# Optimization experiments

Measured on AMD Instinct MI355X. Metric: run time of the kernel, lower is better.

The kernel has to match this reference:

```python
import jax, jax.numpy as jnp
import numpy as np

NUM_NODES_G1 = 60000
NUM_NODES_G2 = 50000
NUM_REL = 16
NUM_BASES = 4
DIM = 128  # node_dim == hidden_dim == final_dim
L_COMMON = 100


def _concept_layer(x, edge_index):
    # Gather-based concept propagation: x_i <- x_i + mean_{j in N(i)} x_j
    src, dst = edge_index[0], edge_index[1]
    n = x.shape[0]
    agg = jax.ops.segment_sum(x[src], dst, num_segments=n)
    deg = jax.ops.segment_sum(jnp.ones((src.shape[0],), x.dtype), dst, num_segments=n)
    return x + agg / jnp.clip(deg, 1.0)[:, None]


def _rgcn_layer(x, edge_index, edge_type, basis, comp, root, bias):
    # Basis-decomposed RGCN: out_i = x_i @ root + bias + sum_r (1/|N_i^r|) sum_{j in N_i^r} x_j @ W_r,
    # W_r = sum_b comp[r,b] * basis[b]. Reorder: scatter comp-weighted x[src] per basis, then one GEMM per basis.
    src, dst = edge_index[0], edge_index[1]
    n = x.shape[0]
    e = src.shape[0]
    seg = dst * NUM_REL + edge_type  # per-(node, relation) bucket
    cnt = jax.ops.segment_sum(jnp.ones((e,), x.dtype), seg, num_segments=n * NUM_REL)
    norm = 1.0 / jnp.clip(cnt, 1.0)
    coef = comp[edge_type] * norm[seg][:, None]  # [E, B]
    xsrc = x[src]  # [E, D] -- dominant gather traffic
    out = x @ root + bias
    for b in range(NUM_BASES):  # small fixed loop over bases
        agg_b = jax.ops.segment_sum(xsrc * coef[:, b:b + 1], dst, num_segments=n)
        out = out + agg_b @ basis[b]
    return out


def setup_inputs() -> dict:
    key = jax.random.key(0)
    ks = jax.random.split(key, 16)
    e2, e1 = 800000, 800000
    return {
        "edge_index_g2": jax.random.randint(ks[0], (2, e2), 0, NUM_NODES_G2),
        "edge_type_g2": jax.random.randint(ks[1], (e2,), 0, NUM_REL),
        "edge_index_g1": jax.random.randint(ks[2], (2, e1), 0, NUM_NODES_G1),
        "left_common": jax.random.randint(ks[3], (L_COMMON,), 0, NUM_NODES_G1),
        "all_node_embedding": jax.random.normal(ks[4], (NUM_NODES_G1, DIM), jnp.float32),
        "basis1": jax.random.normal(ks[5], (NUM_BASES, DIM, DIM), jnp.float32) * 0.05,
        "comp1": jax.random.normal(ks[6], (NUM_REL, NUM_BASES), jnp.float32),
        "root1": jax.random.normal(ks[7], (DIM, DIM), jnp.float32) * 0.05,
        "bias1": jnp.zeros((DIM,), jnp.float32),
        "basis2": jax.random.normal(ks[8], (NUM_BASES, DIM, DIM), jnp.float32) * 0.05,
        "comp2": jax.random.normal(ks[9], (NUM_REL, NUM_BASES), jnp.float32),
        "root2": jax.random.normal(ks[10], (DIM, DIM), jnp.float32) * 0.05,
        "bias2": jnp.zeros((DIM,), jnp.float32),
        "weights": jax.random.uniform(ks[11], (DIM, 1), jnp.float32),
    }


def reference(edge_index_g2, edge_type_g2, edge_index_g1, left_common,
              all_node_embedding, basis1, comp1, root1, bias1,
              basis2, comp2, root2, bias2, weights):
    x_g1 = jax.nn.relu(_concept_layer(all_node_embedding, edge_index_g1))
    x = x_g1[:NUM_NODES_G2]
    x = _rgcn_layer(x, edge_index_g2, edge_type_g2, basis1, comp1, root1, bias1)
    x = jax.nn.relu(x)  # relu_use == 1
    x_g2 = _rgcn_layer(x, edge_index_g2, edge_type_g2, basis2, comp2, root2, bias2)
    ty = x_g1[left_common]  # [L, D]
    # mul_def outer elementwise product followed by matmul with weights collapses to one contraction:
    # logits[n,l] = sum_d x_g2[n,d] * ty[l,d] * w[d]
    logits = jnp.einsum('nd,ld,d->nl', x_g2, ty, weights[:, 0])
    return jax.nn.softmax(logits, axis=1)
```

## Files before the change

### kernel.cpp

```cpp
#include <hip/hip_runtime.h>
#include <hip/hip_bf16.h>
#include <math.h>

#define N1 60000
#define N2 50000
#define DIM 128
#define NREL 16
#define NB 4
#define LCOM 100
#define LPAD 112

typedef __attribute__((ext_vector_type(8))) short short8;
typedef __attribute__((ext_vector_type(4))) float f32x4;
typedef __attribute__((ext_vector_type(4))) _Float16 half4;

__device__ __forceinline__ float bf2f(unsigned short u) {
    union { unsigned int i; float f; } c; c.i = ((unsigned int)u) << 16; return c.f;
}
__device__ __forceinline__ unsigned short f2bf(float f) {
    union { float f; unsigned int i; } c; c.f = f;
    unsigned int r = c.i + 0x7FFF + ((c.i >> 16) & 1);
    return (unsigned short)(r >> 16);
}
__device__ __forceinline__ void split8(float4 a, float4 b, short8& h, short8& l) {
    float f[8] = {a.x, a.y, a.z, a.w, b.x, b.y, b.z, b.w};
#pragma unroll
    for (int j = 0; j < 8; j++) {
        unsigned short hh = f2bf(f[j]);
        h[j] = (short)hh;
        l[j] = (short)f2bf(f[j] - bf2f(hh));
    }
}

__global__ __launch_bounds__(256) void k_prelude(
        const int* __restrict__ ei1, int E1, int* __restrict__ deg1, int HB1,
        const int* __restrict__ ei2, int E2, int* __restrict__ deg2, int HB2,
        const float* __restrict__ root1, const float* __restrict__ basis1,
        unsigned short* __restrict__ Wh1, unsigned short* __restrict__ Wl1,
        const float* __restrict__ root2, const float* __restrict__ basis2,
        unsigned short* __restrict__ Wh2, unsigned short* __restrict__ Wl2, int PB,
        const float* __restrict__ emb, _Float16* __restrict__ embh, int n4) {
    int b = blockIdx.x;
    if (b < HB1) {
        int e0 = b * 1024 + threadIdx.x;
#pragma unroll
        for (int j = 0; j < 4; j++) {
            int e = e0 + j * 256;
            if (e < E1) atomicAdd(deg1 + ei1[E1 + e], 1);
        }
    } else if (b < HB1 + HB2) {
        int e0 = (b - HB1) * 1024 + threadIdx.x;
#pragma unroll
        for (int j = 0; j < 4; j++) {
            int e = e0 + j * 256;
            if (e < E2) atomicAdd(deg2 + ei2[E2 + e], 1);
        }
    } else if (b < HB1 + HB2 + PB) {
        int t = (b - HB1 - HB2) * 256 + threadIdx.x;
        if (t < 2 * 640 * 128) {
            int which = t >= 640 * 128;
            int tt = which ? t - 640 * 128 : t;
            const float* root = which ? root2 : root1;
            const float* basis = which ? basis2 : basis1;
            unsigned short* Wh = which ? Wh2 : Wh1;
            unsigned short* Wl = which ? Wl2 : Wl1;
            int k = tt >> 7, n = tt & 127;
            float v = (k < 128) ? root[k * 128 + n] : basis[(k - 128) * 128 + n];
            unsigned short h = f2bf(v);
            Wh[n * 640 + k] = h;
            Wl[n * 640 + k] = f2bf(v - bf2f(h));
        }
    } else {
        int i = (b - HB1 - HB2 - PB) * 256 + threadIdx.x;
        if (i < n4) {
            float4 v = ((const float4*)emb)[i];
            half4 o = {(_Float16)v.x, (_Float16)v.y, (_Float16)v.z, (_Float16)v.w};
            ((half4*)embh)[i] = o;
        }
    }
}

__global__ __launch_bounds__(256) void k_scan_p1m(const int* __restrict__ inA, int nA, int nbA,
                                                  int* __restrict__ bsumA,
                                                  const int* __restrict__ inB, int nB,
                                                  int* __restrict__ bsumB) {
    __shared__ int red[256];
    const int* in; int n; int* bsum; int b;
    if ((int)blockIdx.x < nbA) { in = inA; n = nA; bsum = bsumA; b = blockIdx.x; }
    else { in = inB; n = nB; bsum = bsumB; b = blockIdx.x - nbA; }
    int base = b * 1024;
    int tid = threadIdx.x;
    int s = 0;
#pragma unroll
    for (int j = 0; j < 4; j++) {
        int i = base + tid * 4 + j;
        if (i < n) s += in[i];
    }
    red[tid] = s;
    __syncthreads();
    for (int d = 128; d; d >>= 1) {
        if (tid < d) red[tid] += red[tid + d];
        __syncthreads();
    }
    if (tid == 0) bsum[b] = red[0];
}

__global__ __launch_bounds__(64) void k_scan_p2m(const int* __restrict__ bsumA, int* __restrict__ boffA,
                                                 int* __restrict__ offA, int nbA, int nA,
                                                 const int* __restrict__ bsumB, int* __restrict__ boffB,
                                                 int* __restrict__ offB, int nbB, int nB) {
    __shared__ int s[64];
    const int* bsum; int* boff; int* off; int nb; int n;
    if (blockIdx.x == 0) { bsum = bsumA; boff = boffA; off = offA; nb = nbA; n = nA; }
    else { bsum = bsumB; boff = boffB; off = offB; nb = nbB; n = nB; }
    int tid = threadIdx.x;
    int v = (tid < nb) ? bsum[tid] : 0;
    s[tid] = v;
    __syncthreads();
    for (int d = 1; d < 64; d <<= 1) {
        int t = (tid >= d) ? s[tid - d] : 0;
        __syncthreads();
        s[tid] += t;
        __syncthreads();
    }
    if (tid < nb) boff[tid] = s[tid] - v;
    if (tid == 63) off[n] = s[63];
}

__global__ __launch_bounds__(256) void k_scan_p3m(const int* __restrict__ inA, const int* __restrict__ boffA,
                                                  int* __restrict__ offA, int* __restrict__ curA,
                                                  int nA, int nbA,
                                                  const int* __restrict__ inB, const int* __restrict__ boffB,
                                                  int* __restrict__ offB, int* __restrict__ curB, int nB) {
    __shared__ int red[256];
    const int* in; const int* boff; int* off; int* cur; int n; int b;
    if ((int)blockIdx.x < nbA) { in = inA; boff = boffA; off = offA; cur = curA; n = nA; b = blockIdx.x; }
    else { in = inB; boff = boffB; off = offB; cur = curB; n = nB; b = blockIdx.x - nbA; }
    int base = b * 1024;
    int tid = threadIdx.x;
    int v[4];
    int s = 0;
#pragma unroll
    for (int j = 0; j < 4; j++) {
        int i = base + tid * 4 + j;
        v[j] = (i < n) ? in[i] : 0;
        s += v[j];
    }
    red[tid] = s;
    __syncthreads();
    for (int d = 1; d < 256; d <<= 1) {
        int t = (tid >= d) ? red[tid - d] : 0;
        __syncthreads();
        red[tid] += t;
        __syncthreads();
    }
    int run = boff[b] + red[tid] - s;
#pragma unroll
    for (int j = 0; j < 4; j++) {
        int i = base + tid * 4 + j;
        if (i < n) {
            off[i] = run; cur[i] = run;
            run += v[j];
        }
    }
}

__global__ void k_scat1(const int* __restrict__ ei, int E, int* __restrict__ cur,
                        int* __restrict__ elist) {
    int e0 = blockIdx.x * 1024 + threadIdx.x;
#pragma unroll
    for (int j = 0; j < 4; j++) {
        int e = e0 + j * 256;
        if (e < E) {
            int pos = atomicAdd(cur + ei[E + e], 1);
            elist[pos] = ei[e];
        }
    }
}

__global__ __launch_bounds__(256) void k_mix(
        const _Float16* __restrict__ embh, const float* __restrict__ emb,
        const int* __restrict__ off1, const int* __restrict__ elist1,
        float* __restrict__ xg1, _Float16* __restrict__ xg1h, int CONC_B,
        const int* __restrict__ ei2, const int* __restrict__ et2, int E2,
        int* __restrict__ cur2, int* __restrict__ elist2, int SC2_B,
        const int* __restrict__ lc, const float* __restrict__ w,
        unsigned short* __restrict__ tyh, unsigned short* __restrict__ tyl) {
    int b = blockIdx.x;
    if (b < CONC_B) {
        int node = b * 4 + (threadIdx.x >> 6);
        int lane = threadIdx.x & 63;
        if (node >= N2) return;
        int half = lane >> 5, d4 = (lane & 31) * 4;
        int s0 = off1[node], s1 = off1[node + 1];
        float4 acc = {0.f, 0.f, 0.f, 0.f};
        int i = s0;
        for (; i + 4 <= s1; i += 4) {
            int sa = elist1[i + half];
            int sb = elist1[i + 2 + half];
            half4 ha = *(const half4*)(embh + (size_t)sa * DIM + d4);
            half4 hb = *(const half4*)(embh + (size_t)sb * DIM + d4);
            acc.x += (float)ha[0] + (float)hb[0];
            acc.y += (float)ha[1] + (float)hb[1];
            acc.z += (float)ha[2] + (float)hb[2];
            acc.w += (float)ha[3] + (float)hb[3];
        }
        for (; i < s1; i += 2) {
            int e = i + half;
            bool ok = e < s1;
            int s = elist1[ok ? e : i];
            half4 hv = *(const half4*)(embh + (size_t)s * DIM + d4);
            if (ok) {
                acc.x += (float)hv[0]; acc.y += (float)hv[1];
                acc.z += (float)hv[2]; acc.w += (float)hv[3];
            }
        }
        acc.x += __shfl_xor(acc.x, 32, 64);
        acc.y += __shfl_xor(acc.y, 32, 64);
        acc.z += __shfl_xor(acc.z, 32, 64);
        acc.w += __shfl_xor(acc.w, 32, 64);
        if (half == 0) {
            float inv = 1.0f / (float)max(s1 - s0, 1);
            float4 e = *(const float4*)(emb + (size_t)node * DIM + d4);
            float4 o = {fmaxf(e.x + acc.x * inv, 0.f), fmaxf(e.y + acc.y * inv, 0.f),
                        fmaxf(e.z + acc.z * inv, 0.f), fmaxf(e.w + acc.w * inv, 0.f)};
            *(float4*)(xg1 + (size_t)node * DIM + d4) = o;
            half4 oh = {(_Float16)o.x, (_Float16)o.y, (_Float16)o.z, (_Float16)o.w};
            *(half4*)(xg1h + (size_t)node * DIM + d4) = oh;
        }
    } else if (b < CONC_B + SC2_B) {
        int e0 = (b - CONC_B) * 1024 + threadIdx.x;
#pragma unroll
        for (int j = 0; j < 4; j++) {
            int e = e0 + j * 256;
            if (e < E2) {
                int pos = atomicAdd(cur2 + ei2[E2 + e], 1);
                elist2[pos] = (ei2[e] << 4) | et2[e];
            }
        }
    } else {
        if (threadIdx.x >= 64) return;
        int l = b - CONC_B - SC2_B;
        int lane = threadIdx.x;
        int d0 = lane * 2;
        if (l >= LCOM) {
            ushort2 z = {0, 0};
            *(ushort2*)(tyh + (size_t)l * 128 + d0) = z;
            *(ushort2*)(tyl + (size_t)l * 128 + d0) = z;
            return;
        }
        int row = lc[l];
        int s0 = off1[row], s1 = off1[row + 1];
        float2 acc = {0.f, 0.f};
        for (int i = s0; i < s1; i++) {
            int s = elist1[i];
            float2 v = *(const float2*)(emb + (size_t)s * DIM + lane * 2);
            acc.x += v.x; acc.y += v.y;
        }
        float inv = 1.0f / (float)max(s1 - s0, 1);
        float2 e = *(const float2*)(emb + (size_t)row * DIM + lane * 2);
        float v0 = fmaxf(e.x + acc.x * inv, 0.f) * w[d0];
        float v1 = fmaxf(e.y + acc.y * inv, 0.f) * w[d0 + 1];
        unsigned short h0 = f2bf(v0), h1 = f2bf(v1);
        ushort2 hh = {h0, h1};
        ushort2 ll = {f2bf(v0 - bf2f(h0)), f2bf(v1 - bf2f(h1))};
        *(ushort2*)(tyh + (size_t)l * 128 + d0) = hh;
        *(ushort2*)(tyl + (size_t)l * 128 + d0) = ll;
    }
}

__global__ __launch_bounds__(256) void k_rgcn_gather(const _Float16* __restrict__ xh,
                                                     const int* __restrict__ off,
                                                     const int* __restrict__ elist,
                                                     const float* __restrict__ comp,
                                                     float* __restrict__ agg, int n) {
    __shared__ float scomp[NREL * NB];
    __shared__ float nrmlds[4][NREL];
    if (threadIdx.x < NREL * NB) scomp[threadIdx.x] = comp[threadIdx.x];
    __syncthreads();
    int nb = threadIdx.x >> 6;
    int node = blockIdx.x * 4 + nb;
    int lane = threadIdx.x & 63;
    if (node >= n) return;
    int s0 = off[node], s1 = off[node + 1];
    unsigned long long c0 = 0, c1 = 0;
    for (int i = s0 + lane; i < s1; i += 64) {
        int t = elist[i] & 15;
        if (t < 8) c0 += 1ull << (8 * t); else c1 += 1ull << (8 * (t - 8));
    }
#pragma unroll
    for (int o = 32; o; o >>= 1) {
        c0 += __shfl_xor(c0, o, 64);
        c1 += __shfl_xor(c1, o, 64);
    }
    if (lane < NREL) {
        unsigned int c = (lane < 8) ? (unsigned int)((c0 >> (8 * lane)) & 255)
                                    : (unsigned int)((c1 >> (8 * (lane - 8))) & 255);
        nrmlds[nb][lane] = 1.0f / (float)max(c, 1u);
    }
    int half = lane >> 5, d4 = (lane & 31) * 4;
    float4 a0 = {0, 0, 0, 0}, a1 = a0, a2 = a0, a3 = a0;
    int i = s0;
#define RG_EDGE(E_IDX, GATE)                                                   \
    {                                                                          \
        int p = elist[E_IDX];                                                  \
        int s = p >> 4, t = p & 15;                                            \
        float nr = nrmlds[nb][t] * (GATE);                                     \
        float4 cf = *(const float4*)(scomp + t * 4);                           \
        half4 hv = *(const half4*)(xh + (size_t)s * DIM + d4);                 \
        float4 v = {(float)hv[0], (float)hv[1], (float)hv[2], (float)hv[3]};   \
        float c0_ = cf.x * nr, c1_ = cf.y * nr, c2_ = cf.z * nr, c3_ = cf.w * nr; \
        a0.x = fmaf(c0_, v.x, a0.x); a0.y = fmaf(c0_, v.y, a0.y);              \
        a0.z = fmaf(c0_, v.z, a0.z); a0.w = fmaf(c0_, v.w, a0.w);              \
        a1.x = fmaf(c1_, v.x, a1.x); a1.y = fmaf(c1_, v.y, a1.y);              \
        a1.z = fmaf(c1_, v.z, a1.z); a1.w = fmaf(c1_, v.w, a1.w);              \
        a2.x = fmaf(c2_, v.x, a2.x); a2.y = fmaf(c2_, v.y, a2.y);              \
        a2.z = fmaf(c2_, v.z, a2.z); a2.w = fmaf(c2_, v.w, a2.w);              \
        a3.x = fmaf(c3_, v.x, a3.x); a3.y = fmaf(c3_, v.y, a3.y);              \
        a3.z = fmaf(c3_, v.z, a3.z); a3.w = fmaf(c3_, v.w, a3.w);              \
    }
    for (; i + 4 <= s1; i += 4) {
        RG_EDGE(i + half, 1.0f);
        RG_EDGE(i + 2 + half, 1.0f);
    }
    for (; i < s1; i += 2) {
        int e = i + half;
        bool ok = e < s1;
        int ei_ = ok ? e : i;
        RG_EDGE(ei_, ok ? 1.0f : 0.0f);
    }
#undef RG_EDGE
    a0.x += __shfl_xor(a0.x, 32, 64); a0.y += __shfl_xor(a0.y, 32, 64);
    a0.z += __shfl_xor(a0.z, 32, 64); a0.w += __shfl_xor(a0.w, 32, 64);
    a1.x += __shfl_xor(a1.x, 32, 64); a1.y += __shfl_xor(a1.y, 32, 64);
    a1.z += __shfl_xor(a1.z, 32, 64); a1.w += __shfl_xor(a1.w, 32, 64);
    a2.x += __shfl_xor(a2.x, 32, 64); a2.y += __shfl_xor(a2.y, 32, 64);
    a2.z += __shfl_xor(a2.z, 32, 64); a2.w += __shfl_xor(a2.w, 32, 64);
    a3.x += __shfl_xor(a3.x, 32, 64); a3.y += __shfl_xor(a3.y, 32, 64);
    a3.z += __shfl_xor(a3.z, 32, 64); a3.w += __shfl_xor(a3.w, 32, 64);
    if (half == 0) {
        float* o = agg + (size_t)node * (NB * DIM) + d4;
        *(float4*)(o + 0 * DIM) = a0;
        *(float4*)(o + 1 * DIM) = a1;
        *(float4*)(o + 2 * DIM) = a2;
        *(float4*)(o + 3 * DIM) = a3;
    }
}

#define LDSK 40
__global__ __launch_bounds__(256) void k_gemm(const float* __restrict__ x,
                                              const float* __restrict__ agg,
                                              const unsigned short* __restrict__ Wh,
                                              const unsigned short* __restrict__ Wl,
                                              const float* __restrict__ bias,
                                              float* __restrict__ out,
                                              _Float16* __restrict__ out_h, int relu) {
    __shared__ __align__(16) short Ah[128 * LDSK];
    __shared__ __align__(16) short Al[128 * LDSK];
    __shared__ __align__(16) short Bh[128 * LDSK];
    __shared__ __align__(16) short Bl[128 * LDSK];
    int tid = threadIdx.x;
    int lane = tid & 63, wid = tid >> 6;
    int wave_m = wid >> 1, wave_n = wid & 1;
    int l15 = lane & 15, quad = lane >> 4;
    int row0 = blockIdx.x * 128;

    int srow = tid >> 1, skh = (tid & 1) * 16;

    f32x4 acc[4][4] = {};
    for (int k0 = 0; k0 < 640; k0 += 32) {
        {
            int rg = row0 + srow;
            float4 q0 = {0, 0, 0, 0}, q1 = q0, q2 = q0, q3 = q0;
            if (rg < N2) {
                const float* src = (k0 < 128) ? (x + (size_t)rg * 128 + k0 + skh)
                                              : (agg + (size_t)rg * 512 + (k0 - 128) + skh);
                q0 = *(const float4*)(src + 0);
                q1 = *(const float4*)(src + 4);
                q2 = *(const float4*)(src + 8);
                q3 = *(const float4*)(src + 12);
            }
            short8 h0, l0, h1, l1;
            split8(q0, q1, h0, l0);
            split8(q2, q3, h1, l1);
            *(short8*)(&Ah[srow * LDSK + skh]) = h0;
            *(short8*)(&Ah[srow * LDSK + skh + 8]) = h1;
            *(short8*)(&Al[srow * LDSK + skh]) = l0;
            *(short8*)(&Al[srow * LDSK + skh + 8]) = l1;
        }
        {
            const unsigned short* sh = Wh + (size_t)srow * 640 + k0 + skh;
            const unsigned short* sl = Wl + (size_t)srow * 640 + k0 + skh;
            *(short8*)(&Bh[srow * LDSK + skh]) = *(const short8*)(sh);
            *(short8*)(&Bh[srow * LDSK + skh + 8]) = *(const short8*)(sh + 8);
            *(short8*)(&Bl[srow * LDSK + skh]) = *(const short8*)(sl);
            *(short8*)(&Bl[srow * LDSK + skh + 8]) = *(const short8*)(sl + 8);
        }
        __syncthreads();
        short8 ah[4], al[4], bh[4], bl[4];
#pragma unroll
        for (int i = 0; i < 4; i++) {
            int ro = (wave_m * 64 + i * 16 + l15) * LDSK + quad * 8;
            ah[i] = *(const short8*)(&Ah[ro]);
            al[i] = *(const short8*)(&Al[ro]);
        }
#pragma unroll
        for (int j = 0; j < 4; j++) {
            int ro = (wave_n * 64 + j * 16 + l15) * LDSK + quad * 8;
            bh[j] = *(const short8*)(&Bh[ro]);
            bl[j] = *(const short8*)(&Bl[ro]);
        }
#pragma unroll
        for (int i = 0; i < 4; i++)
#pragma unroll
            for (int j = 0; j < 4; j++) {
                acc[i][j] = __builtin_amdgcn_mfma_f32_16x16x32_bf16(al[i], bh[j], acc[i][j], 0, 0, 0);
                acc[i][j] = __builtin_amdgcn_mfma_f32_16x16x32_bf16(ah[i], bl[j], acc[i][j], 0, 0, 0);
                acc[i][j] = __builtin_amdgcn_mfma_f32_16x16x32_bf16(ah[i], bh[j], acc[i][j], 0, 0, 0);
            }
        __syncthreads();
    }
#pragma unroll
    for (int j = 0; j < 4; j++) {
        int gcol = wave_n * 64 + j * 16 + l15;
        float bv = bias[gcol];
#pragma unroll
        for (int i = 0; i < 4; i++) {
            int grow_base = row0 + wave_m * 64 + i * 16 + quad * 4;
#pragma unroll
            for (int r = 0; r < 4; r++) {
                int grow = grow_base + r;
                if (grow >= N2) continue;
                float v = acc[i][j][r] + bv;
                if (relu) v = fmaxf(v, 0.f);
                out[(size_t)grow * 128 + gcol] = v;
                if (out_h) out_h[(size_t)grow * 128 + gcol] = (_Float16)v;
            }
        }
    }
}

__global__ __launch_bounds__(256) void k_logits(const float* __restrict__ h2,
                                                const unsigned short* __restrict__ tyh,
                                                const unsigned short* __restrict__ tyl,
                                                float* __restrict__ out, int M) {
    int wid = threadIdx.x >> 6, lane = threadIdx.x & 63;
    int l15 = lane & 15, quad = lane >> 4;
    int row0w = blockIdx.x * 64 + wid * 16;
    int arow = min(row0w + l15, M - 1);
    f32x4 acc[7] = {};
#pragma unroll
    for (int k0 = 0; k0 < 128; k0 += 32) {
        const float* ap = h2 + (size_t)arow * 128 + k0 + quad * 8;
        float4 q0 = *(const float4*)(ap);
        float4 q1 = *(const float4*)(ap + 4);
        short8 ah, al;
        split8(q0, q1, ah, al);
#pragma unroll
        for (int j = 0; j < 7; j++) {
            size_t bo = (size_t)(j * 16 + l15) * 128 + k0 + quad * 8;
            short8 bh = *(const short8*)(tyh + bo);
            short8 bl = *(const short8*)(tyl + bo);
            acc[j] = __builtin_amdgcn_mfma_f32_16x16x32_bf16(al, bh, acc[j], 0, 0, 0);
            acc[j] = __builtin_amdgcn_mfma_f32_16x16x32_bf16(ah, bl, acc[j], 0, 0, 0);
            acc[j] = __builtin_amdgcn_mfma_f32_16x16x32_bf16(ah, bh, acc[j], 0, 0, 0);
        }
    }
    bool v6 = (l15 < LCOM - 96);
#pragma unroll
    for (int r = 0; r < 4; r++) {
        int grow = row0w + quad * 4 + r;
        float m = -INFINITY;
#pragma unroll
        for (int j = 0; j < 6; j++) m = fmaxf(m, acc[j][r]);
        if (v6) m = fmaxf(m, acc[6][r]);
        m = fmaxf(m, __shfl_xor(m, 8, 64));
        m = fmaxf(m, __shfl_xor(m, 4, 64));
        m = fmaxf(m, __shfl_xor(m, 2, 64));
        m = fmaxf(m, __shfl_xor(m, 1, 64));
        float e[7];
        float s = 0.f;
#pragma unroll
        for (int j = 0; j < 6; j++) { e[j] = __expf(acc[j][r] - m); s += e[j]; }
        e[6] = v6 ? __expf(acc[6][r] - m) : 0.f;
        s += e[6];
        s += __shfl_xor(s, 8, 64);
        s += __shfl_xor(s, 4, 64);
        s += __shfl_xor(s, 2, 64);
        s += __shfl_xor(s, 1, 64);
        float inv = 1.0f / s;
        if (grow < M) {
#pragma unroll
            for (int j = 0; j < 6; j++) out[(size_t)grow * LCOM + j * 16 + l15] = e[j] * inv;
            if (v6) out[(size_t)grow * LCOM + 96 + l15] = e[6] * inv;
        }
    }
}

extern "C" void kernel_launch(void* const* d_in, const int* in_sizes, int n_in,
                              void* d_out, int out_size, void* d_ws, size_t ws_size,
                              hipStream_t stream) {
    const int* ei2 = (const int*)d_in[0];
    const int* et2 = (const int*)d_in[1];
    const int* ei1 = (const int*)d_in[2];
    const int* lc = (const int*)d_in[3];
    const float* emb = (const float*)d_in[4];
    const float* basis1 = (const float*)d_in[5];
    const float* comp1 = (const float*)d_in[6];
    const float* root1 = (const float*)d_in[7];
    const float* bias1 = (const float*)d_in[8];
    const float* basis2 = (const float*)d_in[9];
    const float* comp2 = (const float*)d_in[10];
    const float* root2 = (const float*)d_in[11];
    const float* bias2 = (const float*)d_in[12];
    const float* wts = (const float*)d_in[13];
    float* out = (float*)d_out;
    int E2 = in_sizes[0] / 2, E1 = in_sizes[2] / 2;

    float* ws = (float*)d_ws;
    float* xg1 = ws;
    float* h1 = xg1 + 6400000;
    float* agg = h1 + 6400000;
    _Float16* emb_h = (_Float16*)(agg + 25600000);
    unsigned short* tyh = (unsigned short*)(emb_h + 7680000);
    unsigned short* tyl = tyh + LPAD * 128;
    unsigned short* Wh1 = tyl + LPAD * 128;
    unsigned short* Wl1 = Wh1 + 81920;
    unsigned short* Wh2 = Wl1 + 81920;
    unsigned short* Wl2 = Wh2 + 81920;
    int* ipool = (int*)(Wl2 + 81920);
    int* deg1 = ipool;
    int* deg2 = deg1 + 60000;
    int* off1 = deg2 + 50000;
    int* cur1 = off1 + 60001;
    int* elist1 = cur1 + 60000;
    int* off2 = elist1 + 800000;
    int* cur2 = off2 + 50001;
    int* elist2 = cur2 + 50000;
    int* bsum1 = elist2 + 800000;
    int* boff1 = bsum1 + 64;
    int* bsum2 = boff1 + 64;
    int* boff2 = bsum2 + 64;
    _Float16* xg1_h = (_Float16*)h1;
    _Float16* h1_h = emb_h;
    float* h2 = xg1;

    const int NB1 = (N1 + 1023) / 1024;
    const int NB2 = (N2 + 1023) / 1024;
    const int HB1 = (E1 + 1023) / 1024;
    const int HB2 = (E2 + 1023) / 1024;
    const int PB = (2 * 640 * 128) / 256;
    const int CB = (N1 * DIM / 4 + 255) / 256;
    const int CONC_B = (N2 + 3) / 4;
    const int SC2_B = HB2;

    hipMemsetAsync(deg1, 0, (60000 + 50000) * sizeof(int), stream);

    k_prelude<<<HB1 + HB2 + PB + CB, 256, 0, stream>>>(
        ei1, E1, deg1, HB1, ei2, E2, deg2, HB2,
        root1, basis1, Wh1, Wl1, root2, basis2, Wh2, Wl2, PB,
        emb, emb_h, N1 * DIM / 4);

    k_scan_p1m<<<NB1 + NB2, 256, 0, stream>>>(deg1, N1, NB1, bsum1, deg2, N2, bsum2);
    k_scan_p2m<<<2, 64, 0, stream>>>(bsum1, boff1, off1, NB1, N1, bsum2, boff2, off2, NB2, N2);
    k_scan_p3m<<<NB1 + NB2, 256, 0, stream>>>(deg1, boff1, off1, cur1, N1, NB1,
                                              deg2, boff2, off2, cur2, N2);

    k_scat1<<<HB1, 256, 0, stream>>>(ei1, E1, cur1, elist1);

    k_mix<<<CONC_B + SC2_B + LPAD, 256, 0, stream>>>(
        emb_h, emb, off1, elist1, xg1, xg1_h, CONC_B,
        ei2, et2, E2, cur2, elist2, SC2_B,
        lc, wts, tyh, tyl);

    k_rgcn_gather<<<CONC_B, 256, 0, stream>>>(xg1_h, off2, elist2, comp1, agg, N2);
    k_gemm<<<(N2 + 127) / 128, 256, 0, stream>>>(xg1, agg, Wh1, Wl1, bias1, h1, h1_h, 1);

    k_rgcn_gather<<<CONC_B, 256, 0, stream>>>(h1_h, off2, elist2, comp2, agg, N2);
    k_gemm<<<(N2 + 127) / 128, 256, 0, stream>>>(h1, agg, Wh2, Wl2, bias2, h2, (_Float16*)nullptr, 0);

    k_logits<<<(N2 + 63) / 64, 256, 0, stream>>>(h2, tyh, tyl, out, N2);
}
```

Before: 561.2 us.

## Widen gather loads to 16-byte fp16 vectors and move graph-2 scatter earlier

The concept-propagation and RGCN gather kernels now have each lane load 8 fp16 values (16 bytes) and split each wave into 4 edge groups instead of 2. This gives fewer, wider memory transactions per neighbour row and more edges in flight per iteration. The graph-2 edge scatter moves out of the mix kernel into a combined scatter kernel with graph-1, which shrinks the mix launch. The cost is a larger register footprint (32 accumulators in the RGCN gather) and an extra shuffle-reduction step.

```diff
diff --git a/kernel.cpp b/kernel.cpp
--- a/kernel.cpp
+++ b/kernel.cpp
@@ -13,6 +13,7 @@
 typedef __attribute__((ext_vector_type(8))) short short8;
 typedef __attribute__((ext_vector_type(4))) float f32x4;
 typedef __attribute__((ext_vector_type(4))) _Float16 half4;
+typedef __attribute__((ext_vector_type(8))) _Float16 half8;
 
 __device__ __forceinline__ float bf2f(unsigned short u) {
     union { unsigned int i; float f; } c; c.i = ((unsigned int)u) << 16; return c.f;
@@ -165,15 +166,30 @@
     }
 }
 
-__global__ void k_scat1(const int* __restrict__ ei, int E, int* __restrict__ cur,
-                        int* __restrict__ elist) {
-    int e0 = blockIdx.x * 1024 + threadIdx.x;
-#pragma unroll
-    for (int j = 0; j < 4; j++) {
-        int e = e0 + j * 256;
-        if (e < E) {
-            int pos = atomicAdd(cur + ei[E + e], 1);
-            elist[pos] = ei[e];
+__global__ __launch_bounds__(256) void k_scat(const int* __restrict__ ei1, int E1,
+                                              int* __restrict__ cur1, int* __restrict__ elist1, int HB1,
+                                              const int* __restrict__ ei2, const int* __restrict__ et2,
+                                              int E2, int* __restrict__ cur2, int* __restrict__ elist2) {
+    int b = blockIdx.x;
+    if (b < HB1) {
+        int e0 = b * 1024 + threadIdx.x;
+#pragma unroll
+        for (int j = 0; j < 4; j++) {
+            int e = e0 + j * 256;
+            if (e < E1) {
+                int pos = atomicAdd(cur1 + ei1[E1 + e], 1);
+                elist1[pos] = ei1[e];
+            }
+        }
+    } else {
+        int e0 = (b - HB1) * 1024 + threadIdx.x;
+#pragma unroll
+        for (int j = 0; j < 4; j++) {
+            int e = e0 + j * 256;
+            if (e < E2) {
+                int pos = atomicAdd(cur2 + ei2[E2 + e], 1);
+                elist2[pos] = (ei2[e] << 4) | et2[e];
+            }
         }
     }
 }
@@ -182,8 +198,6 @@
         const _Float16* __restrict__ embh, const float* __restrict__ emb,
         const int* __restrict__ off1, const int* __restrict__ elist1,
         float* __restrict__ xg1, _Float16* __restrict__ xg1h, int CONC_B,
-        const int* __restrict__ ei2, const int* __restrict__ et2, int E2,
-        int* __restrict__ cur2, int* __restrict__ elist2, int SC2_B,
         const int* __restrict__ lc, const float* __restrict__ w,
         unsigned short* __restrict__ tyh, unsigned short* __restrict__ tyl) {
     int b = blockIdx.x;
@@ -191,56 +205,66 @@
         int node = b * 4 + (threadIdx.x >> 6);
         int lane = threadIdx.x & 63;
         if (node >= N2) return;
-        int half = lane >> 5, d4 = (lane & 31) * 4;
+        int quad = lane >> 4, d8 = (lane & 15) * 8;
         int s0 = off1[node], s1 = off1[node + 1];
-        float4 acc = {0.f, 0.f, 0.f, 0.f};
+        float acc[8] = {};
         int i = s0;
-        for (; i + 4 <= s1; i += 4) {
-            int sa = elist1[i + half];
-            int sb = elist1[i + 2 + half];
-            half4 ha = *(const half4*)(embh + (size_t)sa * DIM + d4);
-            half4 hb = *(const half4*)(embh + (size_t)sb * DIM + d4);
-            acc.x += (float)ha[0] + (float)hb[0];
-            acc.y += (float)ha[1] + (float)hb[1];
-            acc.z += (float)ha[2] + (float)hb[2];
-            acc.w += (float)ha[3] + (float)hb[3];
-        }
-        for (; i < s1; i += 2) {
-            int e = i + half;
+        for (; i + 8 <= s1; i += 8) {
+            int sa = elist1[i + quad];
+            int sb = elist1[i + 4 + quad];
+            half8 ha = *(const half8*)(embh + (size_t)sa * DIM + d8);
+            half8 hb = *(const half8*)(embh + (size_t)sb * DIM + d8);
+#pragma unroll
+            for (int j = 0; j < 8; j++) acc[j] += (float)ha[j] + (float)hb[j];
+        }
+        if (i + 4 <= s1) {
+            int sa = elist1[i + quad];
+            half8 ha = *(const half8*)(embh + (size_t)sa * DIM + d8);
+#pragma unroll
+            for (int j = 0; j < 8; j++) acc[j] += (float)ha[j];
+            i += 4;
+        }
+        if (i < s1) {
+            int e = i + quad;
             bool ok = e < s1;
             int s = elist1[ok ? e : i];
-            half4 hv = *(const half4*)(embh + (size_t)s * DIM + d4);
+            half8 hv = *(const half8*)(embh + (size_t)s * DIM + d8);
             if (ok) {
-                acc.x += (float)hv[0]; acc.y += (float)hv[1];
-                acc.z += (float)hv[2]; acc.w += (float)hv[3];
+#pragma unroll
+                for (int j = 0; j < 8; j++) acc[j] += (float)hv[j];
             }
         }
-        acc.x += __shfl_xor(acc.x, 32, 64);
-        acc.y += __shfl_xor(acc.y, 32, 64);
-        acc.z += __shfl_xor(acc.z, 32, 64);
-        acc.w += __shfl_xor(acc.w, 32, 64);
-        if (half == 0) {
+#pragma unroll
+        for (int j = 0; j < 8; j++) {
+            acc[j] += __shfl_xor(acc[j], 16, 64);
+            acc[j] += __shfl_xor(acc[j], 32, 64);
+        }
+        if (quad == 0) {
             float inv = 1.0f / (float)max(s1 - s0, 1);
-            float4 e = *(const float4*)(emb + (size_t)node * DIM + d4);
-            float4 o = {fmaxf(e.x + acc.x * inv, 0.f), fmaxf(e.y + acc.y * inv, 0.f),
-                        fmaxf(e.z + acc.z * inv, 0.f), fmaxf(e.w + acc.w * inv, 0.f)};
-            *(float4*)(xg1 + (size_t)node * DIM + d4) = o;
-            half4 oh = {(_Float16)o.x, (_Float16)o.y, (_Float16)o.z, (_Float16)o.w};
-            *(half4*)(xg1h + (size_t)node * DIM + d4) = oh;
-        }
-    } else if (b < CONC_B + SC2_B) {
-        int e0 = (b - CONC_B) * 1024 + threadIdx.x;
-#pragma unroll
-        for (int j = 0; j < 4; j++) {
-            int e = e0 + j * 256;
-            if (e < E2) {
-                int pos = atomicAdd(cur2 + ei2[E2 + e], 1);
-                elist2[pos] = (ei2[e] << 4) | et2[e];
-            }
+            const float* ep = emb + (size_t)node * DIM + d8;
+            float4 e0 = *(const float4*)(ep);
+            float4 e1 = *(const float4*)(ep + 4);
+            float o[8];
+            o[0] = fmaxf(e0.x + acc[0] * inv, 0.f);
+            o[1] = fmaxf(e0.y + acc[1] * inv, 0.f);
+            o[2] = fmaxf(e0.z + acc[2] * inv, 0.f);
+            o[3] = fmaxf(e0.w + acc[3] * inv, 0.f);
+            o[4] = fmaxf(e1.x + acc[4] * inv, 0.f);
+            o[5] = fmaxf(e1.y + acc[5] * inv, 0.f);
+            o[6] = fmaxf(e1.z + acc[6] * inv, 0.f);
+            o[7] = fmaxf(e1.w + acc[7] * inv, 0.f);
+            float4 w0 = {o[0], o[1], o[2], o[3]};
+            float4 w1 = {o[4], o[5], o[6], o[7]};
+            *(float4*)(xg1 + (size_t)node * DIM + d8) = w0;
+            *(float4*)(xg1 + (size_t)node * DIM + d8 + 4) = w1;
+            half8 oh;
+#pragma unroll
+            for (int j = 0; j < 8; j++) oh[j] = (_Float16)o[j];
+            *(half8*)(xg1h + (size_t)node * DIM + d8) = oh;
         }
     } else {
         if (threadIdx.x >= 64) return;
-        int l = b - CONC_B - SC2_B;
+        int l = b - CONC_B;
         int lane = threadIdx.x;
         int d0 = lane * 2;
         if (l >= LCOM) {
@@ -298,52 +322,60 @@
                                     : (unsigned int)((c1 >> (8 * (lane - 8))) & 255);
         nrmlds[nb][lane] = 1.0f / (float)max(c, 1u);
     }
-    int half = lane >> 5, d4 = (lane & 31) * 4;
-    float4 a0 = {0, 0, 0, 0}, a1 = a0, a2 = a0, a3 = a0;
+    int quad = lane >> 4, d8 = (lane & 15) * 8;
+    float a[4][8] = {};
+#define RGE(P, GATE)                                                           \
+    {                                                                          \
+        int s_ = (P) >> 4, t_ = (P) & 15;                                      \
+        float nr_ = nrmlds[nb][t_] * (GATE);                                   \
+        float4 cf_ = *(const float4*)(scomp + t_ * 4);                         \
+        half8 hv_ = *(const half8*)(xh + (size_t)s_ * DIM + d8);               \
+        float c0_ = cf_.x * nr_, c1_ = cf_.y * nr_;                            \
+        float c2_ = cf_.z * nr_, c3_ = cf_.w * nr_;                            \
+        _Pragma("unroll")                                                      \
+        for (int j = 0; j < 8; j++) {                                          \
+            float v_ = (float)hv_[j];                                          \
+            a[0][j] = fmaf(c0_, v_, a[0][j]);                                  \
+            a[1][j] = fmaf(c1_, v_, a[1][j]);                                  \
+            a[2][j] = fmaf(c2_, v_, a[2][j]);                                  \
+            a[3][j] = fmaf(c3_, v_, a[3][j]);                                  \
+        }                                                                      \
+    }
     int i = s0;
-#define RG_EDGE(E_IDX, GATE)                                                   \
-    {                                                                          \
-        int p = elist[E_IDX];                                                  \
-        int s = p >> 4, t = p & 15;                                            \
-        float nr = nrmlds[nb][t] * (GATE);                                     \
-        float4 cf = *(const float4*)(scomp + t * 4);                           \
-        half4 hv = *(const half4*)(xh + (size_t)s * DIM + d4);                 \
-        float4 v = {(float)hv[0], (float)hv[1], (float)hv[2], (float)hv[3]};   \
-        float c0_ = cf.x * nr, c1_ = cf.y * nr, c2_ = cf.z * nr, c3_ = cf.w * nr; \
-        a0.x = fmaf(c0_, v.x, a0.x); a0.y = fmaf(c0_, v.y, a0.y);              \
-        a0.z = fmaf(c0_, v.z, a0.z); a0.w = fmaf(c0_, v.w, a0.w);              \
-        a1.x = fmaf(c1_, v.x, a1.x); a1.y = fmaf(c1_, v.y, a1.y);              \
-        a1.z = fmaf(c1_, v.z, a1.z); a1.w = fmaf(c1_, v.w, a1.w);              \
-        a2.x = fmaf(c2_, v.x, a2.x); a2.y = fmaf(c2_, v.y, a2.y);              \
-        a2.z = fmaf(c2_, v.z, a2.z); a2.w = fmaf(c2_, v.w, a2.w);              \
-        a3.x = fmaf(c3_, v.x, a3.x); a3.y = fmaf(c3_, v.y, a3.y);              \
-        a3.z = fmaf(c3_, v.z, a3.z); a3.w = fmaf(c3_, v.w, a3.w);              \
-    }
-    for (; i + 4 <= s1; i += 4) {
-        RG_EDGE(i + half, 1.0f);
-        RG_EDGE(i + 2 + half, 1.0f);
-    }
-    for (; i < s1; i += 2) {
-        int e = i + half;
+    for (; i + 8 <= s1; i += 8) {
+        int pa = elist[i + quad];
+        int pb = elist[i + 4 + quad];
+        RGE(pa, 1.0f);
+        RGE(pb, 1.0f);
+    }
+    if (i + 4 <= s1) {
+        int pa = elist[i + quad];
+        RGE(pa, 1.0f);
+        i += 4;
+    }
+    if (i < s1) {
+        int e = i + quad;
         bool ok = e < s1;
-        int ei_ = ok ? e : i;
-        RG_EDGE(ei_, ok ? 1.0f : 0.0f);
-    }
-#undef RG_EDGE
-    a0.x += __shfl_xor(a0.x, 32, 64); a0.y += __shfl_xor(a0.y, 32, 64);
-    a0.z += __shfl_xor(a0.z, 32, 64); a0.w += __shfl_xor(a0.w, 32, 64);
-    a1.x += __shfl_xor(a1.x, 32, 64); a1.y += __shfl_xor(a1.y, 32, 64);
-    a1.z += __shfl_xor(a1.z, 32, 64); a1.w += __shfl_xor(a1.w, 32, 64);
-    a2.x += __shfl_xor(a2.x, 32, 64); a2.y += __shfl_xor(a2.y, 32, 64);
-    a2.z += __shfl_xor(a2.z, 32, 64); a2.w += __shfl_xor(a2.w, 32, 64);
-    a3.x += __shfl_xor(a3.x, 32, 64); a3.y += __shfl_xor(a3.y, 32, 64);
-    a3.z += __shfl_xor(a3.z, 32, 64); a3.w += __shfl_xor(a3.w, 32, 64);
-    if (half == 0) {
-        float* o = agg + (size_t)node * (NB * DIM) + d4;
-        *(float4*)(o + 0 * DIM) = a0;
-        *(float4*)(o + 1 * DIM) = a1;
-        *(float4*)(o + 2 * DIM) = a2;
-        *(float4*)(o + 3 * DIM) = a3;
+        int pa = elist[ok ? e : i];
+        RGE(pa, ok ? 1.0f : 0.0f);
+    }
+#undef RGE
+#pragma unroll
+    for (int bb = 0; bb < 4; bb++)
+#pragma unroll
+        for (int j = 0; j < 8; j++) {
+            a[bb][j] += __shfl_xor(a[bb][j], 16, 64);
+            a[bb][j] += __shfl_xor(a[bb][j], 32, 64);
+        }
+    if (quad == 0) {
+        float* o = agg + (size_t)node * (NB * DIM) + d8;
+#pragma unroll
+        for (int bb = 0; bb < 4; bb++) {
+            float4 v0 = {a[bb][0], a[bb][1], a[bb][2], a[bb][3]};
+            float4 v1 = {a[bb][4], a[bb][5], a[bb][6], a[bb][7]};
+            *(float4*)(o + bb * DIM) = v0;
+            *(float4*)(o + bb * DIM + 4) = v1;
+        }
     }
 }
 
@@ -552,7 +584,6 @@
     const int PB = (2 * 640 * 128) / 256;
     const int CB = (N1 * DIM / 4 + 255) / 256;
     const int CONC_B = (N2 + 3) / 4;
-    const int SC2_B = HB2;
 
     hipMemsetAsync(deg1, 0, (60000 + 50000) * sizeof(int), stream);
 
@@ -566,11 +597,11 @@
     k_scan_p3m<<<NB1 + NB2, 256, 0, stream>>>(deg1, boff1, off1, cur1, N1, NB1,
                                               deg2, boff2, off2, cur2, N2);
 
-    k_scat1<<<HB1, 256, 0, stream>>>(ei1, E1, cur1, elist1);
-
-    k_mix<<<CONC_B + SC2_B + LPAD, 256, 0, stream>>>(
+    k_scat<<<HB1 + HB2, 256, 0, stream>>>(ei1, E1, cur1, elist1, HB1,
+                                          ei2, et2, E2, cur2, elist2);
+
+    k_mix<<<CONC_B + LPAD, 256, 0, stream>>>(
         emb_h, emb, off1, elist1, xg1, xg1_h, CONC_B,
-        ei2, et2, E2, cur2, elist2, SC2_B,
         lc, wts, tyh, tyl);
 
     k_rgcn_gather<<<CONC_B, 256, 0, stream>>>(xg1_h, off2, elist2, comp1, agg, N2);
```

After: 591.9 us. +5.5%, slower.
